# Optimization experiments

Measured on AMD Instinct MI355X. Metric: run time of the kernel, lower is better.

The kernel has to match this reference:

```python
import jax, jax.numpy as jnp
import numpy as np

VOCAB, EMBED, HIDDEN, CH = 500, 80, 512, 128
B, L, T = 128, 784, 256


def setup_inputs() -> dict:
    key = jax.random.key(0)
    ks = jax.random.split(key, 14)
    s = lambda fan_in: 1.0 / np.sqrt(fan_in)
    return {
        "latent_rep": jax.random.normal(ks[0], (B, L, CH), jnp.float32),
        "formulas": jax.random.randint(ks[1], (B, T), 0, VOCAB),
        "embedding": jax.random.normal(ks[2], (VOCAB, EMBED), jnp.float32),
        "W_ih": jax.random.uniform(ks[3], (4 * HIDDEN, HIDDEN + EMBED), jnp.float32, -s(HIDDEN), s(HIDDEN)),
        "b_ih": jax.random.uniform(ks[4], (4 * HIDDEN,), jnp.float32, -s(HIDDEN), s(HIDDEN)),
        "W_hh": jax.random.uniform(ks[5], (4 * HIDDEN, HIDDEN), jnp.float32, -s(HIDDEN), s(HIDDEN)),
        "b_hh": jax.random.uniform(ks[6], (4 * HIDDEN,), jnp.float32, -s(HIDDEN), s(HIDDEN)),
        "Wh": jax.random.uniform(ks[7], (HIDDEN, CH), jnp.float32, -s(CH), s(CH)),
        "bh": jax.random.uniform(ks[8], (HIDDEN,), jnp.float32, -s(CH), s(CH)),
        "Wc": jax.random.uniform(ks[9], (HIDDEN, CH), jnp.float32, -s(CH), s(CH)),
        "bc": jax.random.uniform(ks[10], (HIDDEN,), jnp.float32, -s(CH), s(CH)),
        "Wo": jax.random.uniform(ks[11], (HIDDEN, CH), jnp.float32, -s(CH), s(CH)),
        "bo": jax.random.uniform(ks[12], (HIDDEN,), jnp.float32, -s(CH), s(CH)),
    }


def reference(latent_rep, formulas, embedding, W_ih, b_ih, W_hh, b_hh, Wh, bh, Wc, bc, Wo, bo):
    # init_lstm: tanh(Linear(mean over spatial positions))
    mean_lr = latent_rep.mean(axis=1)                       # [B, C]
    h0 = jnp.tanh(mean_lr @ Wh.T + bh)                       # [B, H]
    c0 = jnp.tanh(mean_lr @ Wc.T + bc)
    o0 = jnp.tanh(mean_lr @ Wo.T + bo)                       # fixed across steps in source

    emb = embedding[formulas]                                # [B, T, E]
    xs = jnp.swapaxes(emb, 0, 1)                             # [T, B, E]

    def step(carry, emb_t):
        h, c = carry
        inp = jnp.concatenate([o0, emb_t], axis=1)           # [B, H+E]
        gates = inp @ W_ih.T + b_ih + h @ W_hh.T + b_hh      # [B, 4H]
        i_g, f_g, g_g, o_g = jnp.split(gates, 4, axis=1)
        c_new = jax.nn.sigmoid(f_g) * c + jax.nn.sigmoid(i_g) * jnp.tanh(g_g)
        h_new = jax.nn.sigmoid(o_g) * jnp.tanh(c_new)
        # dropout in eval mode = identity
        return (h_new, c_new), h_new

    _, hs = jax.lax.scan(step, (h0, c0), xs)                 # hs: [T, B, H]
    return jnp.swapaxes(hs, 0, 1)                            # [B, T, H]
```

## Files before the change

kernel.cpp:

```cpp
#include <hip/hip_runtime.h>
#include <hip/hip_bf16.h>
#include <stdint.h>

typedef unsigned int uint32;
typedef unsigned long long uint64;
typedef __attribute__((ext_vector_type(8))) short short8;
typedef __attribute__((ext_vector_type(4))) float f32x4;

#define NB 128
#define NT 256
#define NH 512
#define NE 80
#define NCH 128
#define NL 784
#define NV 500
#define NG4 2048

#define HB_PAIRS (NB*(NH/2))

__device__ __forceinline__ unsigned short f2bf(float f){
  union { float f; unsigned int i; } v; v.f = f;
  unsigned int r = v.i + 0x7FFFu + ((v.i >> 16) & 1u);
  return (unsigned short)(r >> 16);
}
__device__ __forceinline__ float sigf(float x){ return 1.0f/(1.0f + __expf(-x)); }
__device__ __forceinline__ float tanhfast(float x){ return 1.0f - 2.0f/(__expf(2.0f*x)+1.0f); }

__global__ void k_mean(const float* __restrict__ lat, float* __restrict__ meanv){
  int b = blockIdx.x;
  int tid = threadIdx.x;
  int c4 = tid & 31;
  int part = tid >> 5;
  const float4* row = (const float4*)(lat + (size_t)b*NL*NCH);
  float sx=0.f, sy=0.f, sz=0.f, sw=0.f;
  for (int l=part; l<NL; l+=8){
    float4 v = row[l*32 + c4];
    sx+=v.x; sy+=v.y; sz+=v.z; sw+=v.w;
  }
  __shared__ float red[8][32][4];
  red[part][c4][0]=sx; red[part][c4][1]=sy; red[part][c4][2]=sz; red[part][c4][3]=sw;
  __syncthreads();
  if (part==0){
    float a0=0,a1=0,a2=0,a3=0;
    #pragma unroll
    for (int p=0;p<8;p++){ a0+=red[p][c4][0]; a1+=red[p][c4][1]; a2+=red[p][c4][2]; a3+=red[p][c4][3]; }
    float4 o; o.x=a0*(1.0f/NL); o.y=a1*(1.0f/NL); o.z=a2*(1.0f/NL); o.w=a3*(1.0f/NL);
    ((float4*)meanv)[b*32 + c4] = o;
  }
}

__global__ void k_init(const float* __restrict__ meanv,
    const float* __restrict__ Wh, const float* __restrict__ bh,
    const float* __restrict__ Wc, const float* __restrict__ bc,
    const float* __restrict__ Wo, const float* __restrict__ bo,
    float* __restrict__ c0, float* __restrict__ o0, uint64* __restrict__ hbuf){
  int b = blockIdx.x; int j = threadIdx.x;
  __shared__ unsigned short hsh[NH];
  const float* m = meanv + b*NCH;
  const float4* wh = (const float4*)(Wh + (size_t)j*NCH);
  const float4* wc = (const float4*)(Wc + (size_t)j*NCH);
  const float4* wo = (const float4*)(Wo + (size_t)j*NCH);
  float sh=0.f, sc=0.f, so=0.f;
  for (int c=0; c<NCH/4; c++){
    float4 vh = wh[c], vc = wc[c], vo = wo[c];
    float m0=m[c*4], m1=m[c*4+1], m2=m[c*4+2], m3=m[c*4+3];
    sh += m0*vh.x + m1*vh.y + m2*vh.z + m3*vh.w;
    sc += m0*vc.x + m1*vc.y + m2*vc.z + m3*vc.w;
    so += m0*vo.x + m1*vo.y + m2*vo.z + m3*vo.w;
  }
  float h0 = tanhf(sh + bh[j]);
  c0[b*NH+j] = tanhf(sc + bc[j]);
  o0[b*NH+j] = tanhf(so + bo[j]);
  hsh[j] = f2bf(h0);
  __syncthreads();
  if (j < NH/2){
    uint32 packed = (uint32)hsh[2*j] | ((uint32)hsh[2*j+1] << 16);
    hbuf[(size_t)b*(NH/2) + j] = (uint64)packed;
  }
}

__global__ void k_table(const float* __restrict__ emb,
                        const float* __restrict__ Wih,
                        float* __restrict__ table){
  int v = blockIdx.x;
  int n = blockIdx.y*256 + threadIdx.x;
  const float4* wr = (const float4*)(Wih + (size_t)n*(NH+NE) + NH);
  const float4* er = (const float4*)(emb + v*NE);
  float s = 0.f;
  for (int e4=0; e4<NE/4; e4++){
    float4 w = wr[e4], e = er[e4];
    s += w.x*e.x + w.y*e.y + w.z*e.z + w.w*e.w;
  }
  table[(size_t)v*NG4 + n] = s;
}

__global__ void k_base(const float* __restrict__ o0,
                       const float* __restrict__ Wih,
                       const float* __restrict__ bih,
                       const float* __restrict__ bhh,
                       float* __restrict__ base){
  int b = blockIdx.x;
  int n = blockIdx.y*256 + threadIdx.x;
  const float4* o = (const float4*)(o0 + b*NH);
  const float4* wr = (const float4*)(Wih + (size_t)n*(NH+NE));
  float s = bih[n] + bhh[n];
  for (int k4=0;k4<NH/4;k4++){
    float4 w = wr[k4], v = o[k4];
    s += w.x*v.x + w.y*v.y + w.z*v.z + w.w*v.w;
  }
  base[(size_t)b*NG4 + n] = s;
}

__global__ __launch_bounds__(256, 1) void k_lstm(
    const float* __restrict__ Whh,
    const int* __restrict__ formulas,
    const float* __restrict__ table,
    const float* __restrict__ base,
    const float* __restrict__ c0,
    uint64* hbuf,
    float* __restrict__ out)
{
  int bid = blockIdx.x;
  int g = bid & 7, s = bid >> 3;
  int tid = threadIdx.x;
  int lane = tid & 63, w = tid >> 6;
  int b0 = g*16, u0 = s*32;

  __shared__ __align__(16) char h_lds[16*1024];
  __shared__ float G[16*132 + 4];

  short8 bw[2][16];
  {
    int krow = (lane >> 4) * 8;
    #pragma unroll
    for (int h2=0; h2<2; h2++){
      int c_loc = w*32 + h2*16 + (lane & 15);
      int wrow = (c_loc >> 5)*NH + u0 + (c_loc & 31);
      const float4* p4 = (const float4*)(Whh + (size_t)wrow*NH + krow);
      #pragma unroll
      for (int ks=0; ks<16; ks++){
        float4 lo = p4[ks*8], hi = p4[ks*8+1];
        short8 t;
        t[0]=(short)f2bf(lo.x); t[1]=(short)f2bf(lo.y); t[2]=(short)f2bf(lo.z); t[3]=(short)f2bf(lo.w);
        t[4]=(short)f2bf(hi.x); t[5]=(short)f2bf(hi.y); t[6]=(short)f2bf(hi.z); t[7]=(short)f2bf(hi.w);
        bw[h2][ks] = t;
      }
    }
  }

  int r_e = tid >> 4, up = tid & 15;
  int be = b0 + r_e;
  float cst0 = c0[be*NH + u0 + 2*up];
  float cst1 = c0[be*NH + u0 + 2*up + 1];

  float2 bsv[4];
  #pragma unroll
  for (int gt=0; gt<4; gt++)
    bsv[gt] = *(const float2*)(base + (size_t)be*NG4 + gt*NH + u0 + 2*up);

  float2 tbv[4];
  {
    int tok0 = formulas[be*NT + 0];
    #pragma unroll
    for (int gt=0; gt<4; gt++)
      tbv[gt] = *(const float2*)(table + (size_t)tok0*NG4 + gt*NH + u0 + 2*up);
  }

  int arow = lane & 15;
  int abyte = arow*1024 + ((lane>>4)*8)*2;
  int aswz = (arow & 7) << 4;

  for (int t=0; t<NT; t++){
    uint64* hrd = hbuf + (size_t)(t & 1)*HB_PAIRS;
    uint64* hwr = hbuf + (size_t)((t+1) & 1)*HB_PAIRS;
    const uint32 etag = (uint32)t;

    uint64 vv[16];
    #pragma unroll
    for (int i=0;i<16;i++)
      vv[i] = __hip_atomic_load(&hrd[(size_t)b0*(NH/2) + tid + i*256],
                                __ATOMIC_RELAXED, __HIP_MEMORY_SCOPE_AGENT);
    uint32 stale = 0;
    #pragma unroll
    for (int i=0;i<16;i++) if ((uint32)(vv[i] >> 32) != etag) stale |= 1u << i;
    int guard = 0;
    while (stale && ++guard < (1<<16)){
      #pragma unroll
      for (int i=0;i<16;i++) if (stale & (1u << i))
        vv[i] = __hip_atomic_load(&hrd[(size_t)b0*(NH/2) + tid + i*256],
                                  __ATOMIC_RELAXED, __HIP_MEMORY_SCOPE_AGENT);
      stale = 0;
      #pragma unroll
      for (int i=0;i<16;i++) if ((uint32)(vv[i] >> 32) != etag) stale |= 1u << i;
    }

    #pragma unroll
    for (int i=0;i<16;i++){
      int p = tid + i*256;
      int r = p >> 8, cu = p & 255;
      *(uint32*)(h_lds + ((r*1024 + cu*4) ^ ((r & 7) << 4))) = (uint32)vv[i];
    }
    __syncthreads();

    f32x4 acc0 = {0.f,0.f,0.f,0.f}, acc1 = {0.f,0.f,0.f,0.f};
    #pragma unroll
    for (int ks=0; ks<16; ks++){
      short8 a = *(const short8*)(h_lds + ((abyte + ks*64) ^ aswz));
      acc0 = __builtin_amdgcn_mfma_f32_16x16x32_bf16(a, bw[0][ks], acc0, 0, 0, 0);
      acc1 = __builtin_amdgcn_mfma_f32_16x16x32_bf16(a, bw[1][ks], acc1, 0, 0, 0);
    }

    {
      int rbase = (lane>>4)*4;
      int col0 = (w*2+0)*16 + (lane&15);
      int col1 = (w*2+1)*16 + (lane&15);
      #pragma unroll
      for (int r4=0;r4<4;r4++){
        G[(rbase+r4)*132 + col0] = acc0[r4];
        G[(rbase+r4)*132 + col1] = acc1[r4];
      }
    }
    __syncthreads();

    float hn0, hn1;
    {
      const float* Gr = G + r_e*132 + 2*up;
      float gi0 = Gr[0]   + tbv[0].x + bsv[0].x;
      float gi1 = Gr[1]   + tbv[0].y + bsv[0].y;
      float gf0 = Gr[32]  + tbv[1].x + bsv[1].x;
      float gf1 = Gr[33]  + tbv[1].y + bsv[1].y;
      float gg0 = Gr[64]  + tbv[2].x + bsv[2].x;
      float gg1 = Gr[65]  + tbv[2].y + bsv[2].y;
      float go0 = Gr[96]  + tbv[3].x + bsv[3].x;
      float go1 = Gr[97]  + tbv[3].y + bsv[3].y;
      float cn0 = sigf(gf0)*cst0 + sigf(gi0)*tanhfast(gg0);
      float cn1 = sigf(gf1)*cst1 + sigf(gi1)*tanhfast(gg1);
      cst0 = cn0; cst1 = cn1;
      hn0 = sigf(go0)*tanhfast(cn0);
      hn1 = sigf(go1)*tanhfast(cn1);
    }

    if (t < NT-1){
      uint32 packed = (uint32)f2bf(hn0) | ((uint32)f2bf(hn1) << 16);
      uint64 pv = (uint64)packed | ((uint64)(uint32)(t+1) << 32);
      __hip_atomic_store(&hwr[(size_t)be*(NH/2) + (u0/2 + up)], pv,
                         __ATOMIC_RELAXED, __HIP_MEMORY_SCOPE_AGENT);
    }

    {
      float2 ov; ov.x = hn0; ov.y = hn1;
      *(float2*)(out + ((size_t)be*NT + t)*NH + u0 + 2*up) = ov;
    }
    if (t < NT-1){
      int tokn = formulas[be*NT + t + 1];
      #pragma unroll
      for (int gt=0; gt<4; gt++)
        tbv[gt] = *(const float2*)(table + (size_t)tokn*NG4 + gt*NH + u0 + 2*up);
    }
  }
}

extern "C" void kernel_launch(void* const* d_in, const int* in_sizes, int n_in,
                              void* d_out, int out_size, void* d_ws, size_t ws_size,
                              hipStream_t stream) {
  const float* lat      = (const float*)d_in[0];
  const int*   formulas = (const int*)d_in[1];
  const float* emb      = (const float*)d_in[2];
  const float* Wih      = (const float*)d_in[3];
  const float* bih      = (const float*)d_in[4];
  const float* Whh      = (const float*)d_in[5];
  const float* bhh      = (const float*)d_in[6];
  const float* Wh       = (const float*)d_in[7];
  const float* bh       = (const float*)d_in[8];
  const float* Wc       = (const float*)d_in[9];
  const float* bc       = (const float*)d_in[10];
  const float* Wo       = (const float*)d_in[11];
  const float* bo       = (const float*)d_in[12];
  float* out = (float*)d_out;

  char* ws = (char*)d_ws;
  float* meanv = (float*)ws;  ws += (size_t)NB*NCH*4;
  float* c0    = (float*)ws;  ws += (size_t)NB*NH*4;
  float* o0    = (float*)ws;  ws += (size_t)NB*NH*4;
  float* table = (float*)ws;  ws += (size_t)NV*NG4*4;
  float* base  = (float*)ws;  ws += (size_t)NB*NG4*4;
  uint64* hbuf = (uint64*)ws; ws += (size_t)2*HB_PAIRS*8;

  hipMemsetAsync(hbuf, 0, (size_t)2*HB_PAIRS*8, stream);
  k_mean <<<NB, 256, 0, stream>>>(lat, meanv);
  k_init <<<NB, NH, 0, stream>>>(meanv, Wh, bh, Wc, bc, Wo, bo, c0, o0, hbuf);
  k_table<<<dim3(NV, 8), 256, 0, stream>>>(emb, Wih, table);
  k_base <<<dim3(NB, 8), 256, 0, stream>>>(o0, Wih, bih, bhh, base);
  k_lstm <<<NB, 256, 0, stream>>>(Whh, formulas, table, base, c0, hbuf, out);
}
```

Baseline: 740.7 us.

## Replace per-element epoch tags with per-group counters and use 512-thread LSTM blocks

```diff
diff --git a/kernel.cpp b/kernel.cpp
--- a/kernel.cpp
+++ b/kernel.cpp
@@ -16,7 +16,7 @@
 #define NV 500
 #define NG4 2048
 
-#define HB_PAIRS (NB*(NH/2))
+#define HPAIRS (NB*(NH/2))
 
 __device__ __forceinline__ unsigned short f2bf(float f){
   union { float f; unsigned int i; } v; v.f = f;
@@ -53,7 +53,7 @@
     const float* __restrict__ Wh, const float* __restrict__ bh,
     const float* __restrict__ Wc, const float* __restrict__ bc,
     const float* __restrict__ Wo, const float* __restrict__ bo,
-    float* __restrict__ c0, float* __restrict__ o0, uint64* __restrict__ hbuf){
+    float* __restrict__ c0, float* __restrict__ o0, uint32* __restrict__ hbuf){
   int b = blockIdx.x; int j = threadIdx.x;
   __shared__ unsigned short hsh[NH];
   const float* m = meanv + b*NCH;
@@ -73,10 +73,8 @@
   o0[b*NH+j] = tanhf(so + bo[j]);
   hsh[j] = f2bf(h0);
   __syncthreads();
-  if (j < NH/2){
-    uint32 packed = (uint32)hsh[2*j] | ((uint32)hsh[2*j+1] << 16);
-    hbuf[(size_t)b*(NH/2) + j] = (uint64)packed;
-  }
+  if (j < NH/2)
+    hbuf[(size_t)b*(NH/2) + j] = (uint32)hsh[2*j] | ((uint32)hsh[2*j+1] << 16);
 }
 
 __global__ void k_table(const float* __restrict__ emb,
@@ -111,44 +109,44 @@
   base[(size_t)b*NG4 + n] = s;
 }
 
-__global__ __launch_bounds__(256, 1) void k_lstm(
+__global__ __launch_bounds__(512, 1) void k_lstm(
     const float* __restrict__ Whh,
     const int* __restrict__ formulas,
     const float* __restrict__ table,
     const float* __restrict__ base,
     const float* __restrict__ c0,
-    uint64* hbuf,
+    uint32* hbuf, int* cnt,
     float* __restrict__ out)
 {
   int bid = blockIdx.x;
   int g = bid & 7, s = bid >> 3;
   int tid = threadIdx.x;
   int lane = tid & 63, w = tid >> 6;
-  int b0 = g*16, u0 = s*32;
+  int b0 = g*16, u0 = s*64;
+  int row = lane & 15, hi = lane >> 4;
 
   __shared__ __align__(16) char h_lds[16*1024];
-  __shared__ float G[16*132 + 4];
+  __shared__ float G[16*257 + 8];
 
   short8 bw[2][16];
   {
-    int krow = (lane >> 4) * 8;
     #pragma unroll
     for (int h2=0; h2<2; h2++){
-      int c_loc = w*32 + h2*16 + (lane & 15);
-      int wrow = (c_loc >> 5)*NH + u0 + (c_loc & 31);
-      const float4* p4 = (const float4*)(Whh + (size_t)wrow*NH + krow);
+      int c_loc = w*32 + h2*16 + row;
+      int wrow = (c_loc >> 6)*NH + u0 + (c_loc & 63);
+      const float4* p4 = (const float4*)(Whh + (size_t)wrow*NH);
       #pragma unroll
       for (int ks=0; ks<16; ks++){
-        float4 lo = p4[ks*8], hi = p4[ks*8+1];
+        float4 lo = p4[ks*8 + hi*2], hp = p4[ks*8 + hi*2 + 1];
         short8 t;
         t[0]=(short)f2bf(lo.x); t[1]=(short)f2bf(lo.y); t[2]=(short)f2bf(lo.z); t[3]=(short)f2bf(lo.w);
-        t[4]=(short)f2bf(hi.x); t[5]=(short)f2bf(hi.y); t[6]=(short)f2bf(hi.z); t[7]=(short)f2bf(hi.w);
+        t[4]=(short)f2bf(hp.x); t[5]=(short)f2bf(hp.y); t[6]=(short)f2bf(hp.z); t[7]=(short)f2bf(hp.w);
         bw[h2][ks] = t;
       }
     }
   }
 
-  int r_e = tid >> 4, up = tid & 15;
+  int r_e = tid >> 5, up = tid & 31;
   int be = b0 + r_e;
   float cst0 = c0[be*NH + u0 + 2*up];
   float cst1 = c0[be*NH + u0 + 2*up + 1];
@@ -166,39 +164,36 @@
       tbv[gt] = *(const float2*)(table + (size_t)tok0*NG4 + gt*NH + u0 + 2*up);
   }
 
-  int arow = lane & 15;
-  int abyte = arow*1024 + ((lane>>4)*8)*2;
-  int aswz = (arow & 7) << 4;
+  int sr = tid >> 5;
+  int sc8 = (tid & 31) * 8;
+  int abyte = row*1024 + hi*16;
+  int aswz = (row & 7) << 4;
+
+  int* gcnt = cnt + g*32;
 
   for (int t=0; t<NT; t++){
-    uint64* hrd = hbuf + (size_t)(t & 1)*HB_PAIRS;
-    uint64* hwr = hbuf + (size_t)((t+1) & 1)*HB_PAIRS;
-    const uint32 etag = (uint32)t;
-
-    uint64 vv[16];
-    #pragma unroll
-    for (int i=0;i<16;i++)
-      vv[i] = __hip_atomic_load(&hrd[(size_t)b0*(NH/2) + tid + i*256],
-                                __ATOMIC_RELAXED, __HIP_MEMORY_SCOPE_AGENT);
-    uint32 stale = 0;
-    #pragma unroll
-    for (int i=0;i<16;i++) if ((uint32)(vv[i] >> 32) != etag) stale |= 1u << i;
-    int guard = 0;
-    while (stale && ++guard < (1<<16)){
-      #pragma unroll
-      for (int i=0;i<16;i++) if (stale & (1u << i))
-        vv[i] = __hip_atomic_load(&hrd[(size_t)b0*(NH/2) + tid + i*256],
-                                  __ATOMIC_RELAXED, __HIP_MEMORY_SCOPE_AGENT);
-      stale = 0;
-      #pragma unroll
-      for (int i=0;i<16;i++) if ((uint32)(vv[i] >> 32) != etag) stale |= 1u << i;
-    }
-
-    #pragma unroll
-    for (int i=0;i<16;i++){
-      int p = tid + i*256;
-      int r = p >> 8, cu = p & 255;
-      *(uint32*)(h_lds + ((r*1024 + cu*4) ^ ((r & 7) << 4))) = (uint32)vv[i];
+    const uint32* hrd = hbuf + (size_t)(t & 1)*HPAIRS;
+    uint32*       hwr = hbuf + (size_t)((t+1) & 1)*HPAIRS;
+
+    if (t > 0){
+      int tgt = 8*t, guard = 0;
+      while (__hip_atomic_load(gcnt, __ATOMIC_RELAXED, __HIP_MEMORY_SCOPE_AGENT) < tgt){
+        if (++guard > (1<<20)) break;
+      }
+    }
+
+    {
+      const uint64* dp = (const uint64*)(hrd + (size_t)b0*(NH/2)) + (sr*128 + (sc8 >> 1));
+      uint64 d0 = __hip_atomic_load(dp+0, __ATOMIC_RELAXED, __HIP_MEMORY_SCOPE_AGENT);
+      uint64 d1 = __hip_atomic_load(dp+1, __ATOMIC_RELAXED, __HIP_MEMORY_SCOPE_AGENT);
+      uint64 d2 = __hip_atomic_load(dp+2, __ATOMIC_RELAXED, __HIP_MEMORY_SCOPE_AGENT);
+      uint64 d3 = __hip_atomic_load(dp+3, __ATOMIC_RELAXED, __HIP_MEMORY_SCOPE_AGENT);
+      int bb = sr*1024 + sc8*4;
+      int sw = (sr & 7) << 4;
+      *(uint64*)(h_lds + ((bb +  0) ^ sw)) = d0;
+      *(uint64*)(h_lds + ((bb +  8) ^ sw)) = d1;
+      *(uint64*)(h_lds + ((bb + 16) ^ sw)) = d2;
+      *(uint64*)(h_lds + ((bb + 24) ^ sw)) = d3;
     }
     __syncthreads();
 
@@ -211,28 +206,29 @@
     }
 
     {
-      int rbase = (lane>>4)*4;
-      int col0 = (w*2+0)*16 + (lane&15);
-      int col1 = (w*2+1)*16 + (lane&15);
+      int rbase = hi*4;
+      int col0 = w*32 + row;
+      int col1 = w*32 + 16 + row;
       #pragma unroll
       for (int r4=0;r4<4;r4++){
-        G[(rbase+r4)*132 + col0] = acc0[r4];
-        G[(rbase+r4)*132 + col1] = acc1[r4];
+        G[(rbase+r4)*257 + col0] = acc0[r4];
+        G[(rbase+r4)*257 + col1] = acc1[r4];
       }
     }
     __syncthreads();
 
     float hn0, hn1;
     {
-      const float* Gr = G + r_e*132 + 2*up;
-      float gi0 = Gr[0]   + tbv[0].x + bsv[0].x;
-      float gi1 = Gr[1]   + tbv[0].y + bsv[0].y;
-      float gf0 = Gr[32]  + tbv[1].x + bsv[1].x;
-      float gf1 = Gr[33]  + tbv[1].y + bsv[1].y;
-      float gg0 = Gr[64]  + tbv[2].x + bsv[2].x;
-      float gg1 = Gr[65]  + tbv[2].y + bsv[2].y;
-      float go0 = Gr[96]  + tbv[3].x + bsv[3].x;
-      float go1 = Gr[97]  + tbv[3].y + bsv[3].y;
+      const float* Gr = G + r_e*257;
+      int cu = 2*up;
+      float gi0 = Gr[0*64 + cu]     + tbv[0].x + bsv[0].x;
+      float gi1 = Gr[0*64 + cu + 1] + tbv[0].y + bsv[0].y;
+      float gf0 = Gr[1*64 + cu]     + tbv[1].x + bsv[1].x;
+      float gf1 = Gr[1*64 + cu + 1] + tbv[1].y + bsv[1].y;
+      float gg0 = Gr[2*64 + cu]     + tbv[2].x + bsv[2].x;
+      float gg1 = Gr[2*64 + cu + 1] + tbv[2].y + bsv[2].y;
+      float go0 = Gr[3*64 + cu]     + tbv[3].x + bsv[3].x;
+      float go1 = Gr[3*64 + cu + 1] + tbv[3].y + bsv[3].y;
       float cn0 = sigf(gf0)*cst0 + sigf(gi0)*tanhfast(gg0);
       float cn1 = sigf(gf1)*cst1 + sigf(gi1)*tanhfast(gg1);
       cst0 = cn0; cst1 = cn1;
@@ -242,9 +238,11 @@
 
     if (t < NT-1){
       uint32 packed = (uint32)f2bf(hn0) | ((uint32)f2bf(hn1) << 16);
-      uint64 pv = (uint64)packed | ((uint64)(uint32)(t+1) << 32);
-      __hip_atomic_store(&hwr[(size_t)be*(NH/2) + (u0/2 + up)], pv,
+      __hip_atomic_store(&hwr[(size_t)be*(NH/2) + (u0/2 + up)], packed,
                          __ATOMIC_RELAXED, __HIP_MEMORY_SCOPE_AGENT);
+      __syncthreads();
+      if (tid == 0)
+        __hip_atomic_fetch_add(gcnt, 1, __ATOMIC_RELAXED, __HIP_MEMORY_SCOPE_AGENT);
     }
 
     {
@@ -284,12 +282,13 @@
   float* o0    = (float*)ws;  ws += (size_t)NB*NH*4;
   float* table = (float*)ws;  ws += (size_t)NV*NG4*4;
   float* base  = (float*)ws;  ws += (size_t)NB*NG4*4;
-  uint64* hbuf = (uint64*)ws; ws += (size_t)2*HB_PAIRS*8;
-
-  hipMemsetAsync(hbuf, 0, (size_t)2*HB_PAIRS*8, stream);
+  uint32* hbuf = (uint32*)ws; ws += (size_t)2*HPAIRS*4;
+  int*    cnt  = (int*)ws;    ws += 8*32*4;
+
+  hipMemsetAsync(cnt, 0, 8*32*4, stream);
   k_mean <<<NB, 256, 0, stream>>>(lat, meanv);
   k_init <<<NB, NH, 0, stream>>>(meanv, Wh, bh, Wc, bc, Wo, bo, c0, o0, hbuf);
   k_table<<<dim3(NV, 8), 256, 0, stream>>>(emb, Wih, table);
   k_base <<<dim3(NB, 8), 256, 0, stream>>>(o0, Wih, bih, bhh, base);
-  k_lstm <<<NB, 256, 0, stream>>>(Whh, formulas, table, base, c0, hbuf, out);
-}
+  k_lstm <<<64, 512, 0, stream>>>(Whh, formulas, table, base, c0, hbuf, cnt, out);
+}
```

After: 855.4 us. 1.15x slower.
